# Kernel tuning notes

Measured on AMD Instinct MI355X. Metric: run time of the kernel, lower is better.

The kernel has to match this reference:

```python
import jax, jax.numpy as jnp
import numpy as np

GRAD_WIDTH = 0.5  # PeriodicExponential defaults in sinabs
GRAD_SCALE = 1.0

B, T, C_IN, C_OUT = 100, 500, 300, 500


def setup_inputs() -> dict:
    key = jax.random.key(0)
    k1, k2, k3 = jax.random.split(key, 3)
    x = jax.random.normal(k1, (B, T, C_IN), dtype=jnp.float32)
    W = jax.random.normal(k2, (C_OUT, C_IN), dtype=jnp.float32) / np.sqrt(C_IN).astype(np.float32)
    alpha = jax.random.uniform(k3, (B * C_OUT,), dtype=jnp.float32)  # decay in [0,1)
    return {"x": x, "W": W, "alpha": alpha}


def _periodic_exp_pdf(v_mem, threshold):
    # sinabs.activation.PeriodicExponential surrogate gradient
    vs = v_mem - threshold / 2
    vper = vs - threshold * jnp.floor(vs / threshold)
    vnew = jnp.where(v_mem < threshold, vs, vper)
    return GRAD_SCALE / GRAD_WIDTH * jnp.exp(-jnp.abs(vnew - threshold / 2) / GRAD_WIDTH)


@jax.custom_vjp
def spike_fn(v_pre, threshold):
    # multi-spike: floor(v/theta) spikes when above threshold (max_num_spikes=None)
    return jnp.where(v_pre >= threshold, jnp.floor(v_pre / threshold), 0.0)


def _spike_fwd(v_pre, threshold):
    return spike_fn(v_pre, threshold), (v_pre, threshold)


def _spike_bwd(res, g):
    v_pre, threshold = res
    return (g * _periodic_exp_pdf(v_pre, threshold), jnp.zeros_like(threshold))


spike_fn.defvjp(_spike_fwd, _spike_bwd)


def _lif_forward(x, W, alpha):
    threshold = jnp.ones_like(alpha)
    v_init = jnp.zeros_like(alpha)
    # Linear (no bias): [B,T,Cin] @ [Cout,Cin]^T -> [B,T,Cout]
    x_lin = jnp.einsum('btc,oc->bto', x, W)
    # movedim(1,-1).flatten(0,1) -> neurons [B*Cout], time-major for scan: [T, B*Cout]
    inp = x_lin.transpose(1, 0, 2).reshape(T, B * C_OUT)

    def step(v, x_t):
        v_pre = alpha * v + x_t                      # leaky integrate
        v_pre = jnp.maximum(v_pre, -threshold)       # lower bound min_v_mem = -threshold
        s = spike_fn(v_pre, threshold)               # fire (multi-spike)
        v_post = v_pre - threshold * s               # reset by membrane subtraction
        return v_post, s

    _, spikes = jax.lax.scan(step, v_init, inp)      # spikes: [T, B*Cout]
    # reshape(B, Cout, T).movedim(-1, 1) -> [B, T, Cout]
    return spikes.reshape(T, B, C_OUT).transpose(1, 0, 2)


def reference(x, W, alpha):
    return _lif_forward(x, W, alpha)
```

## Files before the change

### kernel.cpp

```cpp
#include <hip/hip_runtime.h>
#include <hip/hip_bf16.h>
#include <stdint.h>

#define NB 100
#define NT 500
#define CIN 300
#define COUT 500
#define M_TOT (NB * NT)
#define MTILES 391
#define NTILES 4
#define KTILES 10
#define NPANEL (MTILES * KTILES + NTILES * KTILES)
#define WS_NEED ((size_t)NPANEL * 4096 * 4)

__device__ __forceinline__ void gload_lds16(const void* g, void* l) {
    __builtin_amdgcn_global_load_lds(
        (const __attribute__((address_space(1))) unsigned int*)g,
        (__attribute__((address_space(3))) unsigned int*)l,
        16, 0, 0);
}

__global__ __launch_bounds__(256) void split_t(
    const float* __restrict__ X, const float* __restrict__ W, float* __restrict__ ws)
{
    const int bid = blockIdx.x;
    const int tid = threadIdx.x;
    const float* src; int rowbase, nrows, kt;
    if (bid < MTILES * KTILES) {
        src = X; rowbase = (bid / KTILES) * 128; nrows = M_TOT; kt = bid % KTILES;
    } else {
        const int w = bid - MTILES * KTILES;
        src = W; rowbase = (w / KTILES) * 128; nrows = COUT; kt = w % KTILES;
    }
    const int kk = tid >> 3;
    const int m0 = (tid & 7) * 16;
    const int k  = kt * 32 + kk;

    float v[16];
    #pragma unroll
    for (int j = 0; j < 16; ++j) {
        const int row = rowbase + m0 + j;
        v[j] = (row < nrows && k < CIN) ? src[(size_t)row * CIN + k] : 0.f;
    }
    float* out = ws + (size_t)bid * 4096 + (size_t)kk * 128 + m0;
    #pragma unroll
    for (int c = 0; c < 4; ++c)
        *(float4*)(out + c * 4) = make_float4(v[c*4], v[c*4+1], v[c*4+2], v[c*4+3]);
}

__global__ __launch_bounds__(256) void gemm_t(
    const float* __restrict__ ws, float* __restrict__ C)
{
    __shared__ __align__(16) float As[2][32][128];
    __shared__ __align__(16) float Bs[2][32][128];

    const int mtile = blockIdx.x >> 2;
    const int ntile = blockIdx.x & 3;
    const int m0 = mtile * 128, n0 = ntile * 128;

    const int tid  = threadIdx.x;
    const int lane = tid & 63;
    const int wid  = tid >> 6;
    const int wmb  = (wid >> 1) << 6;
    const int wnb  = (wid & 1) << 6;
    const int r4   = (lane >> 3) << 2;
    const int c4   = (lane & 7) << 2;

    const float* Xp = ws + (size_t)(mtile * KTILES) * 4096;
    const float* Wp = ws + (size_t)(MTILES * KTILES + ntile * KTILES) * 4096;

    float acc[8][8];
    #pragma unroll
    for (int i = 0; i < 8; ++i)
        #pragma unroll
        for (int j = 0; j < 8; ++j) acc[i][j] = 0.f;

    auto stage = [&](int buf, int kt) {
        const float* xs = Xp + (size_t)kt * 4096 + tid * 4;
        const float* wsr = Wp + (size_t)kt * 4096 + tid * 4;
        #pragma unroll
        for (int c = 0; c < 4; ++c) {
            gload_lds16(xs + c * 1024, (char*)&As[buf][0][0] + (c * 256 + tid) * 16);
            gload_lds16(wsr + c * 1024, (char*)&Bs[buf][0][0] + (c * 256 + tid) * 16);
        }
    };

    stage(0, 0);
    __syncthreads();

    for (int kt = 0; kt < KTILES; ++kt) {
        const int cur = kt & 1;
        if (kt + 1 < KTILES) stage(cur ^ 1, kt + 1);

        #pragma unroll 8
        for (int k = 0; k < 32; ++k) {
            float4 a0 = *(const float4*)&As[cur][k][wmb + r4];
            float4 a1 = *(const float4*)&As[cur][k][wmb + 32 + r4];
            float4 b0 = *(const float4*)&Bs[cur][k][wnb + c4];
            float4 b1 = *(const float4*)&Bs[cur][k][wnb + 32 + c4];
            float a[8] = {a0.x, a0.y, a0.z, a0.w, a1.x, a1.y, a1.z, a1.w};
            float b[8] = {b0.x, b0.y, b0.z, b0.w, b1.x, b1.y, b1.z, b1.w};
            #pragma unroll
            for (int i = 0; i < 8; ++i)
                #pragma unroll
                for (int j = 0; j < 8; ++j)
                    acc[i][j] += a[i] * b[j];
        }
        __syncthreads();
    }

    #pragma unroll
    for (int h = 0; h < 2; ++h) {
        #pragma unroll
        for (int i = 0; i < 4; ++i) {
            const int m = m0 + wmb + h * 32 + r4 + i;
            if (m >= M_TOT) continue;
            float* cp = C + (size_t)m * COUT;
            const int col0 = n0 + wnb + c4;
            const int col1 = col0 + 32;
            const int ai = h * 4 + i;
            if (col0 < COUT)
                *(float4*)(cp + col0) = make_float4(acc[ai][0], acc[ai][1], acc[ai][2], acc[ai][3]);
            if (col1 < COUT)
                *(float4*)(cp + col1) = make_float4(acc[ai][4], acc[ai][5], acc[ai][6], acc[ai][7]);
        }
    }
}

constexpr int BM = 128, BN = 128, BK = 32;
constexpr int LDA = BM + 4;

__global__ __launch_bounds__(256) void gemm_f32(
    const float* __restrict__ X, const float* __restrict__ W, float* __restrict__ C)
{
    __shared__ float As[BK][LDA];
    __shared__ float Bs[BK][LDA];

    const int mtile = blockIdx.x >> 2;
    const int ntile = blockIdx.x & 3;
    const int m0 = mtile * BM, n0 = ntile * BN;

    const int tid  = threadIdx.x;
    const int lane = tid & 63;
    const int wid  = tid >> 6;
    const int wmb  = (wid >> 1) << 6;
    const int wnb  = (wid & 1) << 6;
    const int r4   = (lane >> 3) << 2;
    const int c4   = (lane & 7) << 2;
    const int lr = tid >> 3;
    const int lk = (tid & 7) << 2;

    float acc[8][8];
    #pragma unroll
    for (int i = 0; i < 8; ++i)
        #pragma unroll
        for (int j = 0; j < 8; ++j) acc[i][j] = 0.f;

    for (int k0 = 0; k0 < CIN; k0 += BK) {
        const int kk = k0 + lk;
        const bool kv = (kk < CIN);
        #pragma unroll
        for (int p = 0; p < 4; ++p) {
            int row = p * 32 + lr;
            int m = m0 + row;
            float4 v = make_float4(0.f, 0.f, 0.f, 0.f);
            if (kv && m < M_TOT) v = *(const float4*)(X + (size_t)m * CIN + kk);
            As[lk + 0][row] = v.x; As[lk + 1][row] = v.y;
            As[lk + 2][row] = v.z; As[lk + 3][row] = v.w;
        }
        #pragma unroll
        for (int p = 0; p < 4; ++p) {
            int row = p * 32 + lr;
            int o = n0 + row;
            float4 v = make_float4(0.f, 0.f, 0.f, 0.f);
            if (kv && o < COUT) v = *(const float4*)(W + (size_t)o * CIN + kk);
            Bs[lk + 0][row] = v.x; Bs[lk + 1][row] = v.y;
            Bs[lk + 2][row] = v.z; Bs[lk + 3][row] = v.w;
        }
        __syncthreads();
        #pragma unroll 8
        for (int k = 0; k < BK; ++k) {
            float4 a0 = *(const float4*)&As[k][wmb + r4];
            float4 a1 = *(const float4*)&As[k][wmb + 32 + r4];
            float4 b0 = *(const float4*)&Bs[k][wnb + c4];
            float4 b1 = *(const float4*)&Bs[k][wnb + 32 + c4];
            float a[8] = {a0.x, a0.y, a0.z, a0.w, a1.x, a1.y, a1.z, a1.w};
            float b[8] = {b0.x, b0.y, b0.z, b0.w, b1.x, b1.y, b1.z, b1.w};
            #pragma unroll
            for (int i = 0; i < 8; ++i)
                #pragma unroll
                for (int j = 0; j < 8; ++j)
                    acc[i][j] += a[i] * b[j];
        }
        __syncthreads();
    }

    #pragma unroll
    for (int h = 0; h < 2; ++h) {
        #pragma unroll
        for (int i = 0; i < 4; ++i) {
            const int m = m0 + wmb + h * 32 + r4 + i;
            if (m >= M_TOT) continue;
            float* cp = C + (size_t)m * COUT;
            const int col0 = n0 + wnb + c4;
            const int col1 = col0 + 32;
            const int ai = h * 4 + i;
            if (col0 < COUT)
                *(float4*)(cp + col0) = make_float4(acc[ai][0], acc[ai][1], acc[ai][2], acc[ai][3]);
            if (col1 < COUT)
                *(float4*)(cp + col1) = make_float4(acc[ai][4], acc[ai][5], acc[ai][6], acc[ai][7]);
        }
    }
}

__global__ __launch_bounds__(256) void lif_scan(
    const float* __restrict__ alpha, float* __restrict__ C)
{
    const int n = blockIdx.x * blockDim.x + threadIdx.x;
    if (n >= NB * COUT) return;
    const int b = n / COUT, o = n % COUT;
    const float a = alpha[n];
    float v = 0.f;
    float* p = C + (size_t)b * NT * COUT + o;

    constexpr int U = 10;
    for (int t0 = 0; t0 < NT; t0 += U) {
        float xl[U];
        #pragma unroll
        for (int u = 0; u < U; ++u) xl[u] = p[(size_t)(t0 + u) * COUT];
        float s[U];
        #pragma unroll
        for (int u = 0; u < U; ++u) {
            float vp = a * v + xl[u];
            vp = fmaxf(vp, -1.f);
            float sp = (vp >= 1.f) ? floorf(vp) : 0.f;
            v = vp - sp;
            s[u] = sp;
        }
        #pragma unroll
        for (int u = 0; u < U; ++u) p[(size_t)(t0 + u) * COUT] = s[u];
    }
}

extern "C" void kernel_launch(void* const* d_in, const int* in_sizes, int n_in,
                              void* d_out, int out_size, void* d_ws, size_t ws_size,
                              hipStream_t stream) {
    const float* X     = (const float*)d_in[0];
    const float* W     = (const float*)d_in[1];
    const float* alpha = (const float*)d_in[2];
    float* C = (float*)d_out;

    if (ws_size >= WS_NEED && d_ws != nullptr) {
        float* ws = (float*)d_ws;
        split_t<<<dim3(NPANEL), dim3(256), 0, stream>>>(X, W, ws);
        gemm_t<<<dim3(MTILES * NTILES), dim3(256), 0, stream>>>(ws, C);
    } else {
        gemm_f32<<<dim3(MTILES * NTILES), dim3(256), 0, stream>>>(X, W, C);
    }

    const int nneur = NB * COUT;
    lif_scan<<<dim3((nneur + 255) / 256), dim3(256), 0, stream>>>(alpha, C);
}
```

Measured before the change: 293.8 us.

## Enlarge GEMM block tile to 256x128 with 16x8 per-thread microtile

The transposed-panel GEMM block tile grows from 128x128 to 256x128, the K-step shrinks from 32 to 16, and each thread now accumulates a 16x8 tile instead of 8x8. The pre-transpose kernel is reworked to emit separately sized A and B panels to match. The aim is more FMAs per LDS load and fewer blocks. In exchange it needs many more accumulator registers, which may lower occupancy, and a 256-row tile wastes more padded rows at the M edge.

Result: slower. 320.7 us (+9.1%).

```diff
diff --git a/kernel.cpp b/kernel.cpp
--- a/kernel.cpp
+++ b/kernel.cpp
@@ -7,11 +7,16 @@
 #define CIN 300
 #define COUT 500
 #define M_TOT (NB * NT)
-#define MTILES 391
-#define NTILES 4
-#define KTILES 10
-#define NPANEL (MTILES * KTILES + NTILES * KTILES)
-#define WS_NEED ((size_t)NPANEL * 4096 * 4)
+#define BMT 256
+#define BNT 128
+#define MTIL 196
+#define NTIL 4
+#define KTIL 20
+#define APAN_F 4096
+#define BPAN_F 2048
+#define A_PANELS (MTIL * KTIL)
+#define B_PANELS (NTIL * KTIL)
+#define WS_NEED (((size_t)A_PANELS * APAN_F + (size_t)B_PANELS * BPAN_F) * 4)
 
 __device__ __forceinline__ void gload_lds16(const void* g, void* l) {
     __builtin_amdgcn_global_load_lds(
@@ -25,38 +30,140 @@
 {
     const int bid = blockIdx.x;
     const int tid = threadIdx.x;
-    const float* src; int rowbase, nrows, kt;
-    if (bid < MTILES * KTILES) {
-        src = X; rowbase = (bid / KTILES) * 128; nrows = M_TOT; kt = bid % KTILES;
+    if (bid < A_PANELS) {
+        const int rowbase = (bid / KTIL) * BMT;
+        const int kt = bid % KTIL;
+        const int kk = tid >> 4;
+        const int m0 = (tid & 15) * 16;
+        const int k  = kt * 16 + kk;
+        float v[16];
+        #pragma unroll
+        for (int j = 0; j < 16; ++j) {
+            const int row = rowbase + m0 + j;
+            v[j] = (row < M_TOT && k < CIN) ? X[(size_t)row * CIN + k] : 0.f;
+        }
+        float* out = ws + (size_t)bid * APAN_F + (size_t)kk * 256 + m0;
+        #pragma unroll
+        for (int c = 0; c < 4; ++c)
+            *(float4*)(out + c * 4) = make_float4(v[c*4], v[c*4+1], v[c*4+2], v[c*4+3]);
     } else {
-        const int w = bid - MTILES * KTILES;
-        src = W; rowbase = (w / KTILES) * 128; nrows = COUT; kt = w % KTILES;
-    }
-    const int kk = tid >> 3;
-    const int m0 = (tid & 7) * 16;
-    const int k  = kt * 32 + kk;
-
-    float v[16];
-    #pragma unroll
-    for (int j = 0; j < 16; ++j) {
-        const int row = rowbase + m0 + j;
-        v[j] = (row < nrows && k < CIN) ? src[(size_t)row * CIN + k] : 0.f;
-    }
-    float* out = ws + (size_t)bid * 4096 + (size_t)kk * 128 + m0;
-    #pragma unroll
-    for (int c = 0; c < 4; ++c)
-        *(float4*)(out + c * 4) = make_float4(v[c*4], v[c*4+1], v[c*4+2], v[c*4+3]);
+        const int wb = bid - A_PANELS;
+        const int colbase = (wb / KTIL) * BNT;
+        const int kt = wb % KTIL;
+        const int kk = tid >> 4;
+        const int m0 = (tid & 15) * 8;
+        const int k  = kt * 16 + kk;
+        float v[8];
+        #pragma unroll
+        for (int j = 0; j < 8; ++j) {
+            const int row = colbase + m0 + j;
+            v[j] = (row < COUT && k < CIN) ? W[(size_t)row * CIN + k] : 0.f;
+        }
+        float* out = ws + (size_t)A_PANELS * APAN_F + (size_t)wb * BPAN_F + (size_t)kk * 128 + m0;
+        *(float4*)(out + 0) = make_float4(v[0], v[1], v[2], v[3]);
+        *(float4*)(out + 4) = make_float4(v[4], v[5], v[6], v[7]);
+    }
 }
 
 __global__ __launch_bounds__(256) void gemm_t(
     const float* __restrict__ ws, float* __restrict__ C)
 {
-    __shared__ __align__(16) float As[2][32][128];
-    __shared__ __align__(16) float Bs[2][32][128];
+    __shared__ __align__(16) float As[2][16][256];
+    __shared__ __align__(16) float Bs[2][16][128];
 
     const int mtile = blockIdx.x >> 2;
     const int ntile = blockIdx.x & 3;
-    const int m0 = mtile * 128, n0 = ntile * 128;
+    const int m0 = mtile * BMT, n0 = ntile * BNT;
+
+    const int tid  = threadIdx.x;
+    const int lane = tid & 63;
+    const int wid  = tid >> 6;
+    const int wmb  = (wid >> 1) << 7;
+    const int wnb  = (wid & 1) << 6;
+    const int ra   = (lane >> 3) << 2;
+    const int ca   = (lane & 7) << 2;
+
+    const float* Ap = ws + (size_t)(mtile * KTIL) * APAN_F;
+    const float* Bp = ws + (size_t)A_PANELS * APAN_F + (size_t)(ntile * KTIL) * BPAN_F;
+
+    float acc[16][8];
+    #pragma unroll
+    for (int i = 0; i < 16; ++i)
+        #pragma unroll
+        for (int j = 0; j < 8; ++j) acc[i][j] = 0.f;
+
+    auto stage = [&](int buf, int kt) {
+        const float* xs = Ap + (size_t)kt * APAN_F + tid * 4;
+        const float* bs = Bp + (size_t)kt * BPAN_F + tid * 4;
+        #pragma unroll
+        for (int c = 0; c < 4; ++c)
+            gload_lds16(xs + c * 1024, (char*)&As[buf][0][0] + (c * 256 + tid) * 16);
+        #pragma unroll
+        for (int c = 0; c < 2; ++c)
+            gload_lds16(bs + c * 1024, (char*)&Bs[buf][0][0] + (c * 256 + tid) * 16);
+    };
+
+    stage(0, 0);
+    __syncthreads();
+
+    for (int kt = 0; kt < KTIL; ++kt) {
+        const int cur = kt & 1;
+        if (kt + 1 < KTIL) stage(cur ^ 1, kt + 1);
+
+        #pragma unroll 4
+        for (int k = 0; k < 16; ++k) {
+            float4 av[4], bv[2];
+            #pragma unroll
+            for (int s = 0; s < 4; ++s)
+                av[s] = *(const float4*)&As[cur][k][wmb + ra + s * 32];
+            #pragma unroll
+            for (int j = 0; j < 2; ++j)
+                bv[j] = *(const float4*)&Bs[cur][k][wnb + ca + j * 32];
+            float a[16] = {av[0].x, av[0].y, av[0].z, av[0].w,
+                           av[1].x, av[1].y, av[1].z, av[1].w,
+                           av[2].x, av[2].y, av[2].z, av[2].w,
+                           av[3].x, av[3].y, av[3].z, av[3].w};
+            float b[8]  = {bv[0].x, bv[0].y, bv[0].z, bv[0].w,
+                           bv[1].x, bv[1].y, bv[1].z, bv[1].w};
+            #pragma unroll
+            for (int i = 0; i < 16; ++i)
+                #pragma unroll
+                for (int j = 0; j < 8; ++j)
+                    acc[i][j] += a[i] * b[j];
+        }
+        __syncthreads();
+    }
+
+    #pragma unroll
+    for (int s = 0; s < 4; ++s) {
+        #pragma unroll
+        for (int i = 0; i < 4; ++i) {
+            const int m = m0 + wmb + s * 32 + ra + i;
+            if (m >= M_TOT) continue;
+            float* cp = C + (size_t)m * COUT;
+            const int col0 = n0 + wnb + ca;
+            const int col1 = col0 + 32;
+            const int ai = s * 4 + i;
+            if (col0 < COUT)
+                *(float4*)(cp + col0) = make_float4(acc[ai][0], acc[ai][1], acc[ai][2], acc[ai][3]);
+            if (col1 < COUT)
+                *(float4*)(cp + col1) = make_float4(acc[ai][4], acc[ai][5], acc[ai][6], acc[ai][7]);
+        }
+    }
+}
+
+constexpr int BM = 128, BN = 128, BK = 32;
+constexpr int LDA = BM + 4;
+
+__global__ __launch_bounds__(256) void gemm_f32(
+    const float* __restrict__ X, const float* __restrict__ W, float* __restrict__ C)
+{
+    __shared__ float As[BK][LDA];
+    __shared__ float Bs[BK][LDA];
+
+    const int mtile = blockIdx.x >> 2;
+    const int ntile = blockIdx.x & 3;
+    const int m0 = mtile * BM, n0 = ntile * BN;
 
     const int tid  = threadIdx.x;
     const int lane = tid & 63;
@@ -65,9 +172,8 @@
     const int wnb  = (wid & 1) << 6;
     const int r4   = (lane >> 3) << 2;
     const int c4   = (lane & 7) << 2;
-
-    const float* Xp = ws + (size_t)(mtile * KTILES) * 4096;
-    const float* Wp = ws + (size_t)(MTILES * KTILES + ntile * KTILES) * 4096;
+    const int lr = tid >> 3;
+    const int lk = (tid & 7) << 2;
 
     float acc[8][8];
     #pragma unroll
@@ -75,29 +181,34 @@
         #pragma unroll
         for (int j = 0; j < 8; ++j) acc[i][j] = 0.f;
 
-    auto stage = [&](int buf, int kt) {
-        const float* xs = Xp + (size_t)kt * 4096 + tid * 4;
-        const float* wsr = Wp + (size_t)kt * 4096 + tid * 4;
-        #pragma unroll
-        for (int c = 0; c < 4; ++c) {
-            gload_lds16(xs + c * 1024, (char*)&As[buf][0][0] + (c * 256 + tid) * 16);
-            gload_lds16(wsr + c * 1024, (char*)&Bs[buf][0][0] + (c * 256 + tid) * 16);
-        }
-    };
-
-    stage(0, 0);
-    __syncthreads();
-
-    for (int kt = 0; kt < KTILES; ++kt) {
-        const int cur = kt & 1;
-        if (kt + 1 < KTILES) stage(cur ^ 1, kt + 1);
-
+    for (int k0 = 0; k0 < CIN; k0 += BK) {
+        const int kk = k0 + lk;
+        const bool kv = (kk < CIN);
+        #pragma unroll
+        for (int p = 0; p < 4; ++p) {
+            int row = p * 32 + lr;
+            int m = m0 + row;
+            float4 v = make_float4(0.f, 0.f, 0.f, 0.f);
+            if (kv && m < M_TOT) v = *(const float4*)(X + (size_t)m * CIN + kk);
+            As[lk + 0][row] = v.x; As[lk + 1][row] = v.y;
+            As[lk + 2][row] = v.z; As[lk + 3][row] = v.w;
+        }
+        #pragma unroll
+        for (int p = 0; p < 4; ++p) {
+            int row = p * 32 + lr;
+            int o = n0 + row;
+            float4 v = make_float4(0.f, 0.f, 0.f, 0.f);
+            if (kv && o < COUT) v = *(const float4*)(W + (size_t)o * CIN + kk);
+            Bs[lk + 0][row] = v.x; Bs[lk + 1][row] = v.y;
+            Bs[lk + 2][row] = v.z; Bs[lk + 3][row] = v.w;
+        }
+        __syncthreads();
         #pragma unroll 8
-        for (int k = 0; k < 32; ++k) {
-            float4 a0 = *(const float4*)&As[cur][k][wmb + r4];
-            float4 a1 = *(const float4*)&As[cur][k][wmb + 32 + r4];
-            float4 b0 = *(const float4*)&Bs[cur][k][wnb + c4];
-            float4 b1 = *(const float4*)&Bs[cur][k][wnb + 32 + c4];
+        for (int k = 0; k < BK; ++k) {
+            float4 a0 = *(const float4*)&As[k][wmb + r4];
+            float4 a1 = *(const float4*)&As[k][wmb + 32 + r4];
+            float4 b0 = *(const float4*)&Bs[k][wnb + c4];
+            float4 b1 = *(const float4*)&Bs[k][wnb + 32 + c4];
             float a[8] = {a0.x, a0.y, a0.z, a0.w, a1.x, a1.y, a1.z, a1.w};
             float b[8] = {b0.x, b0.y, b0.z, b0.w, b1.x, b1.y, b1.z, b1.w};
             #pragma unroll
@@ -127,92 +238,6 @@
     }
 }
 
-constexpr int BM = 128, BN = 128, BK = 32;
-constexpr int LDA = BM + 4;
-
-__global__ __launch_bounds__(256) void gemm_f32(
-    const float* __restrict__ X, const float* __restrict__ W, float* __restrict__ C)
-{
-    __shared__ float As[BK][LDA];
-    __shared__ float Bs[BK][LDA];
-
-    const int mtile = blockIdx.x >> 2;
-    const int ntile = blockIdx.x & 3;
-    const int m0 = mtile * BM, n0 = ntile * BN;
-
-    const int tid  = threadIdx.x;
-    const int lane = tid & 63;
-    const int wid  = tid >> 6;
-    const int wmb  = (wid >> 1) << 6;
-    const int wnb  = (wid & 1) << 6;
-    const int r4   = (lane >> 3) << 2;
-    const int c4   = (lane & 7) << 2;
-    const int lr = tid >> 3;
-    const int lk = (tid & 7) << 2;
-
-    float acc[8][8];
-    #pragma unroll
-    for (int i = 0; i < 8; ++i)
-        #pragma unroll
-        for (int j = 0; j < 8; ++j) acc[i][j] = 0.f;
-
-    for (int k0 = 0; k0 < CIN; k0 += BK) {
-        const int kk = k0 + lk;
-        const bool kv = (kk < CIN);
-        #pragma unroll
-        for (int p = 0; p < 4; ++p) {
-            int row = p * 32 + lr;
-            int m = m0 + row;
-            float4 v = make_float4(0.f, 0.f, 0.f, 0.f);
-            if (kv && m < M_TOT) v = *(const float4*)(X + (size_t)m * CIN + kk);
-            As[lk + 0][row] = v.x; As[lk + 1][row] = v.y;
-            As[lk + 2][row] = v.z; As[lk + 3][row] = v.w;
-        }
-        #pragma unroll
-        for (int p = 0; p < 4; ++p) {
-            int row = p * 32 + lr;
-            int o = n0 + row;
-            float4 v = make_float4(0.f, 0.f, 0.f, 0.f);
-            if (kv && o < COUT) v = *(const float4*)(W + (size_t)o * CIN + kk);
-            Bs[lk + 0][row] = v.x; Bs[lk + 1][row] = v.y;
-            Bs[lk + 2][row] = v.z; Bs[lk + 3][row] = v.w;
-        }
-        __syncthreads();
-        #pragma unroll 8
-        for (int k = 0; k < BK; ++k) {
-            float4 a0 = *(const float4*)&As[k][wmb + r4];
-            float4 a1 = *(const float4*)&As[k][wmb + 32 + r4];
-            float4 b0 = *(const float4*)&Bs[k][wnb + c4];
-            float4 b1 = *(const float4*)&Bs[k][wnb + 32 + c4];
-            float a[8] = {a0.x, a0.y, a0.z, a0.w, a1.x, a1.y, a1.z, a1.w};
-            float b[8] = {b0.x, b0.y, b0.z, b0.w, b1.x, b1.y, b1.z, b1.w};
-            #pragma unroll
-            for (int i = 0; i < 8; ++i)
-                #pragma unroll
-                for (int j = 0; j < 8; ++j)
-                    acc[i][j] += a[i] * b[j];
-        }
-        __syncthreads();
-    }
-
-    #pragma unroll
-    for (int h = 0; h < 2; ++h) {
-        #pragma unroll
-        for (int i = 0; i < 4; ++i) {
-            const int m = m0 + wmb + h * 32 + r4 + i;
-            if (m >= M_TOT) continue;
-            float* cp = C + (size_t)m * COUT;
-            const int col0 = n0 + wnb + c4;
-            const int col1 = col0 + 32;
-            const int ai = h * 4 + i;
-            if (col0 < COUT)
-                *(float4*)(cp + col0) = make_float4(acc[ai][0], acc[ai][1], acc[ai][2], acc[ai][3]);
-            if (col1 < COUT)
-                *(float4*)(cp + col1) = make_float4(acc[ai][4], acc[ai][5], acc[ai][6], acc[ai][7]);
-        }
-    }
-}
-
 __global__ __launch_bounds__(256) void lif_scan(
     const float* __restrict__ alpha, float* __restrict__ C)
 {
@@ -252,10 +277,11 @@
 
     if (ws_size >= WS_NEED && d_ws != nullptr) {
         float* ws = (float*)d_ws;
-        split_t<<<dim3(NPANEL), dim3(256), 0, stream>>>(X, W, ws);
-        gemm_t<<<dim3(MTILES * NTILES), dim3(256), 0, stream>>>(ws, C);
+        split_t<<<dim3(A_PANELS + B_PANELS), dim3(256), 0, stream>>>(X, W, ws);
+        gemm_t<<<dim3(MTIL * NTIL), dim3(256), 0, stream>>>(ws, C);
     } else {
-        gemm_f32<<<dim3(MTILES * NTILES), dim3(256), 0, stream>>>(X, W, C);
+        const int mtiles = (M_TOT + BM - 1) / BM;
+        gemm_f32<<<dim3(mtiles * 4), dim3(256), 0, stream>>>(X, W, C);
     }
 
     const int nneur = NB * COUT;
```

## Use triple-buffered 16-deep K stages with vmcnt-based waits in GEMM

Applied to the files above, without the earlier changes.

Splits each 32-deep K panel into two 16-deep stages and keeps three LDS buffers so loads run two stages ahead of compute. The full __syncthreads is replaced by explicit s_waitcnt vmcnt plus s_barrier, so only the oldest stage's global-to-LDS loads must finish before the barrier. LDS use drops from 64KB to 48KB per block, which may allow more blocks per CU, at the cost of more barriers per K and reliance on exact counting of outstanding vector-memory ops. K=300 uses 19 half-stages, so the padded final 16 rows of the last panel are no longer processed.

Result: no change. 289.4 us (-1.5%).

```diff
diff --git a/kernel.cpp b/kernel.cpp
--- a/kernel.cpp
+++ b/kernel.cpp
@@ -10,6 +10,7 @@
 #define MTILES 391
 #define NTILES 4
 #define KTILES 10
+#define KT16 19
 #define NPANEL (MTILES * KTILES + NTILES * KTILES)
 #define WS_NEED ((size_t)NPANEL * 4096 * 4)
 
@@ -51,8 +52,8 @@
 __global__ __launch_bounds__(256) void gemm_t(
     const float* __restrict__ ws, float* __restrict__ C)
 {
-    __shared__ __align__(16) float As[2][32][128];
-    __shared__ __align__(16) float Bs[2][32][128];
+    __shared__ __align__(16) float As[3][16][128];
+    __shared__ __align__(16) float Bs[3][16][128];
 
     const int mtile = blockIdx.x >> 2;
     const int ntile = blockIdx.x & 3;
@@ -66,8 +67,8 @@
     const int r4   = (lane >> 3) << 2;
     const int c4   = (lane & 7) << 2;
 
-    const float* Xp = ws + (size_t)(mtile * KTILES) * 4096;
-    const float* Wp = ws + (size_t)(MTILES * KTILES + ntile * KTILES) * 4096;
+    const float* Ap = ws + (size_t)(mtile * KTILES) * 4096;
+    const float* Bp = ws + (size_t)(MTILES * KTILES + ntile * KTILES) * 4096;
 
     float acc[8][8];
     #pragma unroll
@@ -76,24 +77,28 @@
         for (int j = 0; j < 8; ++j) acc[i][j] = 0.f;
 
     auto stage = [&](int buf, int kt) {
-        const float* xs = Xp + (size_t)kt * 4096 + tid * 4;
-        const float* wsr = Wp + (size_t)kt * 4096 + tid * 4;
-        #pragma unroll
-        for (int c = 0; c < 4; ++c) {
-            gload_lds16(xs + c * 1024, (char*)&As[buf][0][0] + (c * 256 + tid) * 16);
-            gload_lds16(wsr + c * 1024, (char*)&Bs[buf][0][0] + (c * 256 + tid) * 16);
+        const size_t poff = (size_t)(kt >> 1) * 4096 + (size_t)(kt & 1) * 2048 + tid * 4;
+        const float* xs = Ap + poff;
+        const float* bs = Bp + poff;
+        #pragma unroll
+        for (int c = 0; c < 2; ++c) {
+            gload_lds16(xs + c * 1024, (char*)&As[buf][0][0] + (size_t)(c * 256 + tid) * 16);
+            gload_lds16(bs + c * 1024, (char*)&Bs[buf][0][0] + (size_t)(c * 256 + tid) * 16);
         }
     };
 
     stage(0, 0);
-    __syncthreads();
-
-    for (int kt = 0; kt < KTILES; ++kt) {
-        const int cur = kt & 1;
-        if (kt + 1 < KTILES) stage(cur ^ 1, kt + 1);
+    stage(1, 1);
+    asm volatile("s_waitcnt vmcnt(4)" ::: "memory");
+    __builtin_amdgcn_s_barrier();
+    asm volatile("" ::: "memory");
+
+    for (int kt = 0; kt < KT16; ++kt) {
+        const int cur = kt % 3;
+        if (kt + 2 < KT16) stage((kt + 2) % 3, kt + 2);
 
         #pragma unroll 8
-        for (int k = 0; k < 32; ++k) {
+        for (int k = 0; k < 16; ++k) {
             float4 a0 = *(const float4*)&As[cur][k][wmb + r4];
             float4 a1 = *(const float4*)&As[cur][k][wmb + 32 + r4];
             float4 b0 = *(const float4*)&Bs[cur][k][wnb + c4];
@@ -106,7 +111,13 @@
                 for (int j = 0; j < 8; ++j)
                     acc[i][j] += a[i] * b[j];
         }
-        __syncthreads();
+
+        if (kt < KT16 - 1) {
+            if (kt + 2 < KT16) asm volatile("s_waitcnt vmcnt(4)" ::: "memory");
+            else               asm volatile("s_waitcnt vmcnt(0)" ::: "memory");
+            __builtin_amdgcn_s_barrier();
+            asm volatile("" ::: "memory");
+        }
     }
 
     #pragma unroll
@@ -255,7 +266,7 @@
         split_t<<<dim3(NPANEL), dim3(256), 0, stream>>>(X, W, ws);
         gemm_t<<<dim3(MTILES * NTILES), dim3(256), 0, stream>>>(ws, C);
     } else {
-        gemm_f32<<<dim3(MTILES * NTILES), dim3(256), 0, stream>>>(X, W, C);
+        gemm_f32<<<dim3(MTILES * 4), dim3(256), 0, stream>>>(X, W, C);
     }
 
     const int nneur = NB * COUT;
```
